# Kernel tuning notes

Measured on AMD Instinct MI355X. Metric: run time of the kernel, lower is better.

Reference implementation:

```python
import jax, jax.numpy as jnp
import numpy as np

# Longformer-base-like config, 4 layers, seq 2048, one-sided window 256 (attention_window=512)
B, S, DM, H, L, FF, V, WIN = 1, 2048, 768, 12, 4, 3072, 50265, 256


def _ln(x, s, b):
    m = x.mean(-1, keepdims=True)
    v = ((x - m) ** 2).mean(-1, keepdims=True)
    return (x - m) * jax.lax.rsqrt(v + 1e-5) * s + b


def setup_inputs() -> dict:
    key = jax.random.key(0)
    ks = iter(jax.random.split(key, 48))
    nrm = lambda shape: jax.random.normal(next(ks), shape, jnp.float32) * 0.02
    z = lambda shape: jnp.zeros(shape, jnp.float32)
    o = lambda shape: jnp.ones(shape, jnp.float32)
    return {
        'src': jax.random.randint(next(ks), (B, S), 0, V),
        'mask_src': jnp.ones((B, S), jnp.int32),
        'cluster_sizes': jax.random.randint(next(ks), (B,), 1, 10),
        'emb_word': nrm((V, DM)), 'emb_pos': nrm((S + 2, DM)),
        'ln_emb_s': o((DM,)), 'ln_emb_b': z((DM,)),
        'Wq': nrm((L, DM, DM)), 'bq': z((L, DM)),
        'Wk': nrm((L, DM, DM)), 'bk': z((L, DM)),
        'Wv': nrm((L, DM, DM)), 'bv': z((L, DM)),
        'Wo': nrm((L, DM, DM)), 'bo': z((L, DM)),
        'Wqg': nrm((L, DM, DM)), 'bqg': z((L, DM)),
        'Wkg': nrm((L, DM, DM)), 'bkg': z((L, DM)),
        'Wvg': nrm((L, DM, DM)), 'bvg': z((L, DM)),
        'ln1_s': o((L, DM)), 'ln1_b': z((L, DM)),
        'Wff1': nrm((L, DM, FF)), 'bff1': z((L, FF)),
        'Wff2': nrm((L, FF, DM)), 'bff2': z((L, DM)),
        'ln2_s': o((L, DM)), 'ln2_b': z((L, DM)),
        'Wcls': nrm((DM,)), 'bcls': z(()),
    }


def _encode(src, mask_src, emb_word, emb_pos, ln_emb_s, ln_emb_b,
            Wq, bq, Wk, bk, Wv, bv, Wo, bo, Wqg, bqg, Wkg, bkg, Wvg, bvg,
            ln1_s, ln1_b, Wff1, bff1, Wff2, bff2, ln2_s, ln2_b):
    Dh = DM // H
    NC = S // WIN  # number of query chunks
    NEG = jnp.float32(-1e9)
    scale = jnp.float32(1.0 / np.sqrt(Dh))
    mask_f = mask_src.astype(jnp.float32)

    # RoBERTa-style embeddings (positions offset by padding_idx+1 = 2)
    x = _ln(emb_word[src] + emb_pos[jnp.arange(S) + 2][None], ln_emb_s, ln_emb_b)

    # Banded gather indices: chunk c of W queries sees 3W keys [c*W - W, c*W + 2W)
    idx = jnp.arange(NC)[:, None] * WIN + jnp.arange(3 * WIN)[None, :]  # [NC,3W] into padded seq
    j_abs = idx - WIN                                                   # absolute key positions
    qi = jnp.arange(NC)[:, None] * WIN + jnp.arange(WIN)[None, :]       # [NC,W] absolute query pos
    rel = j_abs[:, None, :] - qi[:, :, None]                            # [NC,W,3W]
    in_band = (jnp.abs(rel) <= WIN) & (j_abs[:, None, :] >= 0) & (j_abs[:, None, :] < S)
    # keys removed from windowed attention: padding tokens and global tokens (position 0)
    key_ok = mask_f * (jnp.arange(S)[None, :] != 0)                     # [B,S]
    kmb = jnp.pad(key_ok, ((0, 0), (WIN, WIN)))[:, idx]                 # [B,NC,3W]
    band_ok = in_band[None, None] & (kmb[:, None, :, None, :] > 0)      # [B,1,NC,W,3W]

    for l in range(L):
        heads = lambda Wm, bm: (x @ Wm[l] + bm[l]).reshape(B, S, H, Dh).transpose(0, 2, 1, 3)
        q = heads(Wq, bq) * scale                                       # [B,H,S,Dh]
        k = heads(Wk, bk)
        v = heads(Wv, bv)
        kb = jnp.pad(k, ((0, 0), (0, 0), (WIN, WIN), (0, 0)))[:, :, idx]  # [B,H,NC,3W,Dh]
        vb = jnp.pad(v, ((0, 0), (0, 0), (WIN, WIN), (0, 0)))[:, :, idx]
        band = jnp.einsum('bhcqd,bhckd->bhcqk', q.reshape(B, H, NC, WIN, Dh), kb)
        band = jnp.where(band_ok, band, NEG)
        # every query also attends the global key (position 0) via the regular k/v
        sg = jnp.einsum('bhsd,bhd->bhs', q, k[:, :, 0])
        sg = jnp.where((mask_f[:, 0] > 0)[:, None, None], sg, NEG).reshape(B, H, NC, WIN, 1)
        probs = jax.nn.softmax(jnp.concatenate([sg, band], axis=-1), axis=-1)
        pg = probs[..., 0].reshape(B, H, S)
        out = jnp.einsum('bhcqk,bhckd->bhcqd', probs[..., 1:], vb).reshape(B, H, S, Dh)
        out = out + pg[..., None] * v[:, :, 0][:, :, None, :]
        # global query token (position 0): full attention using the *_global projections
        qg = ((x[:, 0] @ Wqg[l] + bqg[l]).reshape(B, H, Dh)) * scale
        kg = heads(Wkg, bkg)
        vg = heads(Wvg, bvg)
        sgl = jnp.where(mask_f[:, None, :] > 0, jnp.einsum('bhd,bhsd->bhs', qg, kg), NEG)
        og = jnp.einsum('bhs,bhsd->bhd', jax.nn.softmax(sgl, axis=-1), vg)
        out = out.at[:, :, 0].set(og)
        ctx = out.transpose(0, 2, 1, 3).reshape(B, S, DM)
        x = _ln(x + ctx @ Wo[l] + bo[l], ln1_s[l], ln1_b[l])
        ff = jax.nn.gelu(x @ Wff1[l] + bff1[l], approximate=False) @ Wff2[l] + bff2[l]
        x = _ln(x + ff, ln2_s[l], ln2_b[l])
    return x


def reference(src, mask_src, cluster_sizes, emb_word, emb_pos, ln_emb_s, ln_emb_b,
              Wq, bq, Wk, bk, Wv, bv, Wo, bo, Wqg, bqg, Wkg, bkg, Wvg, bvg,
              ln1_s, ln1_b, Wff1, bff1, Wff2, bff2, ln2_s, ln2_b, Wcls, bcls):
    x = _encode(src, mask_src, emb_word, emb_pos, ln_emb_s, ln_emb_b,
                Wq, bq, Wk, bk, Wv, bv, Wo, bo, Wqg, bqg, Wkg, bkg, Wvg, bvg,
                ln1_s, ln1_b, Wff1, bff1, Wff2, bff2, ln2_s, ln2_b)
    mask0 = mask_src[:, 0].astype(jnp.float32)
    scores = jax.nn.sigmoid(x[:, 0] @ Wcls + bcls) * mask0  # Classifier on CLS embedding
    return scores[:, None], mask_src[:, 0][:, None]
```

## Files before the change

### kernel.cpp

```cpp
#include <hip/hip_runtime.h>
#include <hip/hip_bf16.h>
#include <math.h>

#define S_LEN 2048
#define DMODEL 768
#define NHEAD 12
#define DHEAD 64
#define NLAYER 4
#define FFDIM 3072
#define WINSZ 256

typedef unsigned short u16;
typedef __attribute__((ext_vector_type(8))) short bfrag;
typedef __attribute__((ext_vector_type(4))) float ffrag;

static __device__ __forceinline__ int detect_bf16(const unsigned* flagp) {
    return flagp[0] != 0x3F800000u;
}

static __device__ __forceinline__ float ldin(const void* p, long i, int bf) {
    return bf ? __bfloat162float(((const __hip_bfloat16*)p)[i])
              : ((const float*)p)[i];
}

static __device__ __forceinline__ u16 f2bf(float v) {
    unsigned u = __float_as_uint(v);
    unsigned r = (u + 0x7FFFu + ((u >> 16) & 1u)) >> 16;
    return (u16)r;
}

static __device__ __forceinline__ float bf2f(u16 v) {
    return __uint_as_float((unsigned)v << 16);
}

static __device__ __forceinline__ void async16(const u16* g, u16* l) {
#if __has_builtin(__builtin_amdgcn_global_load_lds)
    __builtin_amdgcn_global_load_lds(
        (const __attribute__((address_space(1))) void*)g,
        (__attribute__((address_space(3))) void*)l, 16, 0, 0);
#else
    *(int4*)l = *(const int4*)g;
#endif
}

static __device__ __forceinline__ void blk_reduce_sum2(float& a, float& b) {
    __shared__ float sred[8];
    #pragma unroll
    for (int off = 32; off; off >>= 1) {
        a += __shfl_down(a, off);
        b += __shfl_down(b, off);
    }
    int lane = threadIdx.x & 63, w = threadIdx.x >> 6;
    if (lane == 0) { sred[w] = a; sred[w + 4] = b; }
    __syncthreads();
    a = sred[0] + sred[1] + sred[2] + sred[3];
    b = sred[4] + sred[5] + sred[6] + sred[7];
    __syncthreads();
}

struct TAllArgs { const void* w[8]; u16* d6; u16* d1; u16* d2; };

__global__ __launch_bounds__(256)
void transpose_all_kernel(TAllArgs args, const unsigned* __restrict__ flagp) {
    int bf = detect_bf16(flagp);
    const long DD = (long)DMODEL * DMODEL;
    const long DF = (long)DMODEL * FFDIM;
    int bid = blockIdx.x;
    const void* srcp; u16* dst; int K, N, n0, k0; long so, dofs;
    if (bid < 3456) {
        int z = bid / 144, t = bid % 144;
        srcp = args.w[z >> 2]; so = (long)(z & 3) * DD;
        dst = args.d6; dofs = (long)z * DD;
        K = DMODEL; N = DMODEL; n0 = (t % 12) * 64; k0 = (t / 12) * 64;
    } else if (bid < 5760) {
        int i = bid - 3456, layer = i / 576, t = i % 576;
        srcp = args.w[6]; so = (long)layer * DF;
        dst = args.d1; dofs = (long)layer * DF;
        K = DMODEL; N = FFDIM; n0 = (t % 48) * 64; k0 = (t / 48) * 64;
    } else {
        int i = bid - 5760, layer = i / 576, t = i % 576;
        srcp = args.w[7]; so = (long)layer * DF;
        dst = args.d2; dofs = (long)layer * DF;
        K = FFDIM; N = DMODEL; n0 = (t % 12) * 64; k0 = (t / 12) * 64;
    }
    __shared__ float t[64][65];
    int tid = threadIdx.x;
    #pragma unroll
    for (int r = 0; r < 16; ++r) {
        int idx = r * 256 + tid;
        int k = idx >> 6, n = idx & 63;
        t[k][n] = ldin(srcp, so + (long)(k0 + k) * N + n0 + n, bf);
    }
    __syncthreads();
    #pragma unroll
    for (int r = 0; r < 4; ++r) {
        int idx = r * 256 + tid;
        int n = idx >> 4, k4 = (idx & 15) * 4;
        ushort4 pk;
        pk.x = f2bf(t[k4 + 0][n]); pk.y = f2bf(t[k4 + 1][n]);
        pk.z = f2bf(t[k4 + 2][n]); pk.w = f2bf(t[k4 + 3][n]);
        *(ushort4*)&dst[dofs + (long)(n0 + n) * K + k0 + k4] = pk;
    }
}

__global__ __launch_bounds__(256)
void embed_kernel(const int* __restrict__ src, const void* __restrict__ emb_word,
                  const void* __restrict__ emb_pos, const void* __restrict__ ln_s,
                  const void* __restrict__ ln_b, float* __restrict__ X,
                  u16* __restrict__ Xb, const unsigned* __restrict__ flagp) {
    int bf = detect_bf16(flagp);
    int s = blockIdx.x;
    int tid = threadIdx.x;
    int tok = src[s];
    float e[3];
    #pragma unroll
    for (int i = 0; i < 3; ++i) {
        int d = tid + i * 256;
        e[i] = ldin(emb_word, (long)tok * DMODEL + d, bf)
             + ldin(emb_pos, (long)(s + 2) * DMODEL + d, bf);
    }
    float sum = e[0] + e[1] + e[2];
    float sq  = e[0]*e[0] + e[1]*e[1] + e[2]*e[2];
    blk_reduce_sum2(sum, sq);
    float mean = sum * (1.0f / DMODEL);
    float var  = sq * (1.0f / DMODEL) - mean * mean;
    float inv  = rsqrtf(var + 1e-5f);
    #pragma unroll
    for (int i = 0; i < 3; ++i) {
        int d = tid + i * 256;
        float v = (e[i] - mean) * inv * ldin(ln_s, d, bf) + ldin(ln_b, d, bf);
        X[(long)s * DMODEL + d] = v;
        Xb[(long)s * DMODEL + d] = f2bf(v);
    }
}

__global__ __launch_bounds__(256)
void ln_res2_kernel(float* __restrict__ X, const float* __restrict__ T0,
                    const float* __restrict__ T1,
                    const void* __restrict__ ln_s, long soff,
                    const void* __restrict__ ln_b, long boff,
                    u16* __restrict__ Xb, const unsigned* __restrict__ flagp,
                    int do_cls, const void* __restrict__ Wcls,
                    const void* __restrict__ bcls, const int* __restrict__ mask_src,
                    void* __restrict__ out) {
    int bf = detect_bf16(flagp);
    int s = blockIdx.x;
    int tid = threadIdx.x;
    float e[3];
    #pragma unroll
    for (int i = 0; i < 3; ++i) {
        long d = (long)s * DMODEL + tid + i * 256;
        e[i] = X[d] + T0[d] + T1[d];
    }
    float sum = e[0] + e[1] + e[2];
    float sq  = e[0]*e[0] + e[1]*e[1] + e[2]*e[2];
    blk_reduce_sum2(sum, sq);
    float mean = sum * (1.0f / DMODEL);
    float var  = sq * (1.0f / DMODEL) - mean * mean;
    float inv  = rsqrtf(var + 1e-5f);
    float v3[3];
    #pragma unroll
    for (int i = 0; i < 3; ++i) {
        int d = tid + i * 256;
        float v = (e[i] - mean) * inv * ldin(ln_s, soff + d, bf) + ldin(ln_b, boff + d, bf);
        v3[i] = v;
        X[(long)s * DMODEL + d] = v;
        Xb[(long)s * DMODEL + d] = f2bf(v);
    }
    if (do_cls && s == 0) {
        float a = 0.0f, dummy = 0.0f;
        #pragma unroll
        for (int i = 0; i < 3; ++i)
            a = fmaf(v3[i], ldin(Wcls, tid + i * 256, bf), a);
        blk_reduce_sum2(a, dummy);
        if (tid == 0) {
            float z = a + ldin(bcls, 0, bf);
            float scr = 1.0f / (1.0f + __expf(-z));
            float mk = (float)mask_src[0];
            scr *= mk;
            if (bf) {
                __hip_bfloat16* o = (__hip_bfloat16*)out;
                o[0] = __float2bfloat16(scr);
                o[1] = __float2bfloat16(mk);
            } else {
                float* o = (float*)out;
                o[0] = scr;
                o[1] = mk;
            }
        }
    }
}

static __device__ __forceinline__ void gemm_body(
    const u16* __restrict__ A, int lda, const u16* __restrict__ Wt, int ldb,
    const void* __restrict__ bias, long boff, int bf,
    float* __restrict__ outF, u16* __restrict__ outB, u16* __restrict__ outBT, int ldt,
    int N, int klen, float alpha, int gelu,
    u16 (*As)[32], u16 (*Bs)[32], int bm, int bn,
    int patch_mode, const u16* __restrict__ ctx0s, long kbeg)
{
    int tid = threadIdx.x;
    int wave = tid >> 6, lane = tid & 63;
    int quad = lane >> 4, l15 = lane & 15;
    int wn = wave * 32;

    int srow = tid >> 2;
    int scol = (tid & 3) * 8;
    const u16* Ag  = A  + (long)(bm + srow) * lda + scol;
    const u16* Bg0 = Wt + (long)(bn + srow) * ldb + scol;
    const u16* Bg1 = Wt + (long)(bn + 64 + srow) * ldb + scol;
    u16* Al  = &As[srow][scol];
    u16* Bl0 = &Bs[srow][scol];
    u16* Bl1 = &Bs[64 + srow][scol];

    ffrag zero = {0.f, 0.f, 0.f, 0.f};
    ffrag acc[4][2];
    #pragma unroll
    for (int mi = 0; mi < 4; ++mi)
        #pragma unroll
        for (int ni = 0; ni < 2; ++ni) acc[mi][ni] = zero;

    for (int k0 = 0; k0 < klen; k0 += 32) {
        __syncthreads();
        async16(Ag + k0, Al);
        async16(Bg0 + k0, Bl0);
        async16(Bg1 + k0, Bl1);
        __syncthreads();
        if (patch_mode) {
            if (bm == 0 && tid < 4) {
                #pragma unroll
                for (int j = 0; j < 8; ++j)
                    As[0][tid * 8 + j] = ctx0s[kbeg + k0 + tid * 8 + j];
            }
            __syncthreads();
        }
        bfrag af[4], bfr[2];
        #pragma unroll
        for (int mi = 0; mi < 4; ++mi)
            af[mi] = *(const bfrag*)&As[mi * 16 + l15][quad * 8];
        #pragma unroll
        for (int ni = 0; ni < 2; ++ni)
            bfr[ni] = *(const bfrag*)&Bs[wn + ni * 16 + l15][quad * 8];
        #pragma unroll
        for (int mi = 0; mi < 4; ++mi)
            #pragma unroll
            for (int ni = 0; ni < 2; ++ni)
                acc[mi][ni] = __builtin_amdgcn_mfma_f32_16x16x32_bf16(
                    af[mi], bfr[ni], acc[mi][ni], 0, 0, 0);
    }

    #pragma unroll
    for (int mi = 0; mi < 4; ++mi) {
        #pragma unroll
        for (int ni = 0; ni < 2; ++ni) {
            int row0 = bm + mi * 16 + quad * 4;
            int col  = bn + wn + ni * 16 + l15;
            float bb = bias ? ldin(bias, boff + col, bf) : 0.0f;
            float v[4];
            #pragma unroll
            for (int i = 0; i < 4; ++i) {
                float x = (acc[mi][ni][i] + bb) * alpha;
                if (gelu) x = 0.5f * x * (1.0f + erff(x * 0.70710678118f));
                v[i] = x;
            }
            if (outF) {
                #pragma unroll
                for (int i = 0; i < 4; ++i) outF[(long)(row0 + i) * N + col] = v[i];
            }
            if (outB) {
                #pragma unroll
                for (int i = 0; i < 4; ++i) outB[(long)(row0 + i) * N + col] = f2bf(v[i]);
            }
            if (outBT) {
                ushort4 pk;
                pk.x = f2bf(v[0]); pk.y = f2bf(v[1]); pk.z = f2bf(v[2]); pk.w = f2bf(v[3]);
                *(ushort4*)&outBT[(long)col * ldt + row0] = pk;
            }
        }
    }
}

__global__ __launch_bounds__(256)
void gemm_one_kernel(const u16* __restrict__ A, int lda, const u16* __restrict__ Wt, int ldb,
                     const void* __restrict__ bias, long boff,
                     float* __restrict__ outF, long ofstride, u16* __restrict__ outB,
                     int N, int klen, float alpha, int gelu,
                     const float* __restrict__ Gml, const float* __restrict__ GO,
                     const unsigned* __restrict__ flagp) {
    __shared__ __align__(16) u16 As[64][32];
    __shared__ __align__(16) u16 Bs[128][32];
    __shared__ __align__(16) u16 ctx0s[DMODEL];
    int patch = (Gml != nullptr);
    int bm = blockIdx.x * 64;
    if (patch && bm == 0) {
        for (int i = threadIdx.x; i < DMODEL; i += 256) {
            int h = i >> 6, d = i & 63;
            float M = -3e38f;
            #pragma unroll
            for (int z = 0; z < 8; ++z) M = fmaxf(M, Gml[((long)h * 8 + z) * 2]);
            float L = 0.f, O = 0.f;
            #pragma unroll
            for (int z = 0; z < 8; ++z) {
                float w = __expf(Gml[((long)h * 8 + z) * 2] - M);
                L += Gml[((long)h * 8 + z) * 2 + 1] * w;
                O = fmaf(GO[((long)h * 8 + z) * DHEAD + d], w, O);
            }
            ctx0s[i] = f2bf(O / L);
        }
    }
    long kbeg = (long)blockIdx.z * klen;
    gemm_body(A + kbeg, lda, Wt + kbeg, ldb,
              blockIdx.z == 0 ? bias : nullptr, boff, detect_bf16(flagp),
              outF ? outF + blockIdx.z * ofstride : nullptr, outB, nullptr, 0,
              N, klen, alpha, gelu, As, Bs, bm, blockIdx.y * 128,
              patch, ctx0s, kbeg);
}

struct Qkv5Args {
    const u16* wt[5];
    const void* bias[5];
    u16* outB[5];
    u16* outBT[5];
};

__global__ __launch_bounds__(256)
void gemm_qkv5_kernel(const u16* __restrict__ A, Qkv5Args args, long boff,
                      const unsigned* __restrict__ flagp) {
    __shared__ __align__(16) u16 As[64][32];
    __shared__ __align__(16) u16 Bs[128][32];
    int z = blockIdx.z;
    float alpha = (z == 0) ? 0.125f : 1.0f;
    gemm_body(A, DMODEL, args.wt[z], DMODEL, args.bias[z], boff, detect_bf16(flagp),
              nullptr, args.outB[z], args.outBT[z], S_LEN,
              DMODEL, DMODEL, alpha, 0,
              As, Bs, blockIdx.x * 64, blockIdx.y * 128, 0, nullptr, 0);
}

struct BandShared {
    u16 Qs[64][72];
    u16 Ks[64][72];
    u16 Vs[64][72];
    float Pb[4][16][68];
    u16 k0s[64];
    u16 v0s[64];
};
struct GattnShared {
    float xs[DMODEL];
    float qs[DHEAD];
    float sc[256];
    float red[4];
    float pt[4][DHEAD];
};
union AttnShared { BandShared b; GattnShared g; };

__global__ __launch_bounds__(256)
void attn_fused_kernel(const u16* __restrict__ Qb, const u16* __restrict__ Kb,
                       const u16* __restrict__ Vtg, u16* __restrict__ CTXb,
                       const float* __restrict__ X, const void* __restrict__ Wqg, long wo,
                       const void* __restrict__ bqg, long bo,
                       const u16* __restrict__ KG, const u16* __restrict__ VG,
                       float* __restrict__ Gml, float* __restrict__ GO,
                       const unsigned* __restrict__ flagp) {
    __shared__ __align__(16) AttnShared sm;
    int bid = blockIdx.x;
    int tid = threadIdx.x;

    if (bid < 384) {
        int qt = bid & 31, h = bid >> 5;
        int q0 = qt * 64;
        int wave = tid >> 6, lane = tid & 63;
        int quad = lane >> 4, l15 = lane & 15;

        {
            int r = tid >> 2, seg = tid & 3;
            const u16* gq = Qb + (long)(q0 + r) * DMODEL + h * DHEAD + seg * 16;
            *(int4*)&sm.b.Qs[r][seg * 16]     = *(const int4*)gq;
            *(int4*)&sm.b.Qs[r][seg * 16 + 8] = *(const int4*)(gq + 8);
            if (tid < 8) *(int4*)&sm.b.k0s[tid * 8] = *(const int4*)(Kb + h * DHEAD + tid * 8);
            if (tid >= 64 && tid < 128) {
                int d = tid - 64;
                sm.b.v0s[d] = Vtg[(long)(h * DHEAD + d) * S_LEN];
            }
        }
        __syncthreads();

        float part = 0.0f;
        #pragma unroll
        for (int j = 0; j < 16; ++j)
            part = fmaf(bf2f(sm.b.Qs[wave * 16 + l15][quad * 16 + j]),
                        bf2f(sm.b.k0s[quad * 16 + j]), part);
        part += __shfl_xor(part, 16);
        part += __shfl_xor(part, 32);
        float m = part, l = 1.0f;

        ffrag O4[4];
        #pragma unroll
        for (int dt = 0; dt < 4; ++dt) {
            float vv = bf2f(sm.b.v0s[dt * 16 + l15]);
            ffrag t = {vv, vv, vv, vv};
            O4[dt] = t;
        }

        bfrag bq[2];
        bq[0] = *(const bfrag*)&sm.b.Qs[wave * 16 + l15][quad * 8];
        bq[1] = *(const bfrag*)&sm.b.Qs[wave * 16 + l15][32 + quad * 8];

        int q_abs = q0 + wave * 16 + l15;
        float (*Pw)[68] = sm.b.Pb[wave];

        for (int t = 0; t < 9; ++t) {
            int jb = q0 - 256 + t * 64;
            if (jb < 0 || jb >= S_LEN) continue;

            __syncthreads();
            {
                int r = tid >> 2, seg = tid & 3;
                const u16* gk = Kb + (long)(jb + r) * DMODEL + h * DHEAD + seg * 16;
                *(int4*)&sm.b.Ks[r][seg * 16]     = *(const int4*)gk;
                *(int4*)&sm.b.Ks[r][seg * 16 + 8] = *(const int4*)(gk + 8);
                const u16* gv = Vtg + (long)(h * DHEAD + r) * S_LEN + jb + seg * 16;
                *(int4*)&sm.b.Vs[r][seg * 16]     = *(const int4*)gv;
                *(int4*)&sm.b.Vs[r][seg * 16 + 8] = *(const int4*)(gv + 8);
            }
            __syncthreads();

            ffrag sa[4];
            #pragma unroll
            for (int mt = 0; mt < 4; ++mt) {
                bfrag a0 = *(const bfrag*)&sm.b.Ks[mt * 16 + l15][quad * 8];
                bfrag a1 = *(const bfrag*)&sm.b.Ks[mt * 16 + l15][32 + quad * 8];
                ffrag z = {0.f, 0.f, 0.f, 0.f};
                z = __builtin_amdgcn_mfma_f32_16x16x32_bf16(a0, bq[0], z, 0, 0, 0);
                z = __builtin_amdgcn_mfma_f32_16x16x32_bf16(a1, bq[1], z, 0, 0, 0);
                sa[mt] = z;
            }

            float mx = -3e38f;
            #pragma unroll
            for (int mt = 0; mt < 4; ++mt) {
                #pragma unroll
                for (int reg = 0; reg < 4; ++reg) {
                    int key = jb + mt * 16 + quad * 4 + reg;
                    int rel = key - q_abs;
                    bool ok = (key >= 1) && (rel >= -WINSZ) && (rel <= WINSZ);
                    float s = ok ? sa[mt][reg] : -1e30f;
                    sa[mt][reg] = s;
                    mx = fmaxf(mx, s);
                }
            }
            mx = fmaxf(mx, __shfl_xor(mx, 16));
            mx = fmaxf(mx, __shfl_xor(mx, 32));
            float m_new = fmaxf(m, mx);
            float alpha = __expf(m - m_new);

            float rs = 0.0f;
            #pragma unroll
            for (int mt = 0; mt < 4; ++mt) {
                #pragma unroll
                for (int reg = 0; reg < 4; ++reg) {
                    float p = __expf(sa[mt][reg] - m_new);
                    sa[mt][reg] = p;
                    rs += p;
                }
            }
            rs += __shfl_xor(rs, 16);
            rs += __shfl_xor(rs, 32);
            l = l * alpha + rs;
            m = m_new;

            #pragma unroll
            for (int mt = 0; mt < 4; ++mt)
                #pragma unroll
                for (int reg = 0; reg < 4; ++reg)
                    Pw[l15][mt * 16 + quad * 4 + reg] = sa[mt][reg];

            float a4[4];
            #pragma unroll
            for (int reg = 0; reg < 4; ++reg)
                a4[reg] = __shfl(alpha, (lane & 48) + quad * 4 + reg);

            bfrag pa[2];
            #pragma unroll
            for (int ks = 0; ks < 2; ++ks) {
                float4 f0 = *(const float4*)&Pw[l15][ks * 32 + quad * 8];
                float4 f1 = *(const float4*)&Pw[l15][ks * 32 + quad * 8 + 4];
                union { bfrag v; short s[8]; } pu;
                pu.s[0] = (short)f2bf(f0.x); pu.s[1] = (short)f2bf(f0.y);
                pu.s[2] = (short)f2bf(f0.z); pu.s[3] = (short)f2bf(f0.w);
                pu.s[4] = (short)f2bf(f1.x); pu.s[5] = (short)f2bf(f1.y);
                pu.s[6] = (short)f2bf(f1.z); pu.s[7] = (short)f2bf(f1.w);
                pa[ks] = pu.v;
            }

            #pragma unroll
            for (int dt = 0; dt < 4; ++dt) {
                bfrag v0f = *(const bfrag*)&sm.b.Vs[dt * 16 + l15][quad * 8];
                bfrag v1f = *(const bfrag*)&sm.b.Vs[dt * 16 + l15][32 + quad * 8];
                ffrag o = O4[dt];
                #pragma unroll
                for (int reg = 0; reg < 4; ++reg) o[reg] *= a4[reg];
                o = __builtin_amdgcn_mfma_f32_16x16x32_bf16(pa[0], v0f, o, 0, 0, 0);
                o = __builtin_amdgcn_mfma_f32_16x16x32_bf16(pa[1], v1f, o, 0, 0, 0);
                O4[dt] = o;
            }
        }

        float l4[4];
        #pragma unroll
        for (int reg = 0; reg < 4; ++reg)
            l4[reg] = __shfl(l, (lane & 48) + quad * 4 + reg);

        #pragma unroll
        for (int dt = 0; dt < 4; ++dt) {
            #pragma unroll
            for (int reg = 0; reg < 4; ++reg) {
                int row = q0 + wave * 16 + quad * 4 + reg;
                CTXb[(long)row * DMODEL + h * DHEAD + dt * 16 + l15] = f2bf(O4[dt][reg] / l4[reg]);
            }
        }
    } else {
        int bf = detect_bf16(flagp);
        int idx = bid - 384;
        int h = idx >> 3, ck = idx & 7;

        for (int i = tid; i < DMODEL; i += 256) sm.g.xs[i] = X[i];
        __syncthreads();
        {
            int d = tid & 63, part = tid >> 6;
            float a = 0.0f;
            for (int k = part * 192; k < part * 192 + 192; ++k)
                a = fmaf(sm.g.xs[k], ldin(Wqg, wo + (long)k * DMODEL + h * DHEAD + d, bf), a);
            sm.g.pt[part][d] = a;
        }
        __syncthreads();
        if (tid < DHEAD)
            sm.g.qs[tid] = ((sm.g.pt[0][tid] + sm.g.pt[1][tid] + sm.g.pt[2][tid] + sm.g.pt[3][tid])
                            + ldin(bqg, bo + h * DHEAD + tid, bf)) * 0.125f;
        __syncthreads();

        int s = ck * 256 + tid;
        const int4* kp = (const int4*)(KG + (long)s * DMODEL + h * DHEAD);
        float dsum = 0.0f;
        #pragma unroll
        for (int i = 0; i < 8; ++i) {
            int4 raw = kp[i];
            const u16* pr = (const u16*)&raw;
            #pragma unroll
            for (int j = 0; j < 8; ++j) dsum = fmaf(sm.g.qs[i * 8 + j], bf2f(pr[j]), dsum);
        }
        sm.g.sc[tid] = dsum;
        float v = dsum;
        #pragma unroll
        for (int off = 32; off; off >>= 1) v = fmaxf(v, __shfl_down(v, off));
        if ((tid & 63) == 0) sm.g.red[tid >> 6] = v;
        __syncthreads();
        float M = fmaxf(fmaxf(sm.g.red[0], sm.g.red[1]), fmaxf(sm.g.red[2], sm.g.red[3]));
        __syncthreads();
        float e = __expf(dsum - M);
        sm.g.sc[tid] = e;
        float sum = e;
        #pragma unroll
        for (int off = 32; off; off >>= 1) sum += __shfl_down(sum, off);
        if ((tid & 63) == 0) sm.g.red[tid >> 6] = sum;
        __syncthreads();
        float L = sm.g.red[0] + sm.g.red[1] + sm.g.red[2] + sm.g.red[3];

        int g = tid >> 6, dd = tid & 63;
        float acc = 0.0f;
        for (int j = g * 64; j < g * 64 + 64; ++j)
            acc = fmaf(sm.g.sc[j], bf2f(VG[(long)(ck * 256 + j) * DMODEL + h * DHEAD + dd]), acc);
        sm.g.pt[g][dd] = acc;
        __syncthreads();
        if (tid < DHEAD)
            GO[((long)h * 8 + ck) * DHEAD + tid] =
                sm.g.pt[0][tid] + sm.g.pt[1][tid] + sm.g.pt[2][tid] + sm.g.pt[3][tid];
        if (tid == 0) {
            Gml[((long)h * 8 + ck) * 2]     = M;
            Gml[((long)h * 8 + ck) * 2 + 1] = L;
        }
    }
}

extern "C" void kernel_launch(void* const* d_in, const int* in_sizes, int n_in,
                              void* d_out, int out_size, void* d_ws, size_t ws_size,
                              hipStream_t stream) {
    (void)in_sizes; (void)n_in; (void)out_size; (void)ws_size;
    const int* src       = (const int*)d_in[0];
    const int* mask_src  = (const int*)d_in[1];
    const void* emb_word = d_in[3];
    const void* emb_pos  = d_in[4];
    const unsigned* flagp = (const unsigned*)d_in[5];
    const void* ln_emb_s = d_in[5];
    const void* ln_emb_b = d_in[6];

    char* base = (char*)d_ws;
    size_t off = 0;
    auto carve = [&](size_t bytes) {
        void* p = base + off;
        off = (off + bytes + 255) & ~(size_t)255;
        return p;
    };
    const long DD = (long)DMODEL * DMODEL;
    const long DF = (long)DMODEL * FFDIM;
    const long SD = (long)S_LEN * DMODEL;
    const long SF = (long)S_LEN * FFDIM;

    u16* W6    = (u16*)carve(6 * NLAYER * DD * 2);
    u16* FF1T  = (u16*)carve(NLAYER * DF * 2);
    u16* FF2T  = (u16*)carve(NLAYER * DF * 2);
    float* X   = (float*)carve(SD * 4);
    float* TMP0 = (float*)carve(SD * 4);
    float* TMP1 = (float*)carve(SD * 4);
    u16* Xb    = (u16*)carve(SD * 2);
    u16* Qb16  = (u16*)carve(SD * 2);
    u16* Kb16  = (u16*)carve(SD * 2);
    u16* Vtg   = (u16*)carve(SD * 2);
    u16* KGb16 = (u16*)carve(SD * 2);
    u16* VGb16 = (u16*)carve(SD * 2);
    u16* CTXb  = (u16*)carve(SD * 2);
    u16* FF1b  = (u16*)carve(SF * 2);
    float* Gml = (float*)carve(NHEAD * 8 * 2 * 4);
    float* GO  = (float*)carve(NHEAD * 8 * DHEAD * 4);

    TAllArgs ta;
    ta.w[0] = d_in[7];  ta.w[1] = d_in[9];  ta.w[2] = d_in[11];
    ta.w[3] = d_in[17]; ta.w[4] = d_in[19]; ta.w[5] = d_in[13];
    ta.w[6] = d_in[23]; ta.w[7] = d_in[25];
    ta.d6 = W6; ta.d1 = FF1T; ta.d2 = FF2T;
    transpose_all_kernel<<<8064, 256, 0, stream>>>(ta, flagp);

    embed_kernel<<<S_LEN, 256, 0, stream>>>(src, emb_word, emb_pos, ln_emb_s, ln_emb_b,
                                            X, Xb, flagp);

    for (int l = 0; l < NLAYER; ++l) {
        long wo  = (long)l * DD;
        long bo  = (long)l * DMODEL;
        long b1o = (long)l * FFDIM;

        Qkv5Args qa;
        qa.wt[0] = W6 + (0L * NLAYER + l) * DD; qa.bias[0] = d_in[8];  qa.outB[0] = Qb16;  qa.outBT[0] = nullptr;
        qa.wt[1] = W6 + (1L * NLAYER + l) * DD; qa.bias[1] = d_in[10]; qa.outB[1] = Kb16;  qa.outBT[1] = nullptr;
        qa.wt[2] = W6 + (2L * NLAYER + l) * DD; qa.bias[2] = d_in[12]; qa.outB[2] = nullptr; qa.outBT[2] = Vtg;
        qa.wt[3] = W6 + (3L * NLAYER + l) * DD; qa.bias[3] = d_in[18]; qa.outB[3] = KGb16; qa.outBT[3] = nullptr;
        qa.wt[4] = W6 + (4L * NLAYER + l) * DD; qa.bias[4] = d_in[20]; qa.outB[4] = VGb16; qa.outBT[4] = nullptr;
        gemm_qkv5_kernel<<<dim3(32, 6, 5), 256, 0, stream>>>(Xb, qa, bo, flagp);

        attn_fused_kernel<<<480, 256, 0, stream>>>(Qb16, Kb16, Vtg, CTXb,
                                                   X, d_in[15], wo, d_in[16], bo,
                                                   KGb16, VGb16, Gml, GO, flagp);

        gemm_one_kernel<<<dim3(32, 6, 2), 256, 0, stream>>>(
            CTXb, DMODEL, W6 + (5L * NLAYER + l) * DD, DMODEL, d_in[14], bo,
            TMP0, SD, nullptr, DMODEL, 384, 1.0f, 0, Gml, GO, flagp);
        ln_res2_kernel<<<S_LEN, 256, 0, stream>>>(X, TMP0, TMP1, d_in[21], bo, d_in[22], bo,
                                                  Xb, flagp, 0, nullptr, nullptr, nullptr, nullptr);

        gemm_one_kernel<<<dim3(32, 24, 1), 256, 0, stream>>>(
            Xb, DMODEL, FF1T + (long)l * DF, DMODEL, d_in[24], b1o,
            nullptr, 0, FF1b, FFDIM, DMODEL, 1.0f, 1, nullptr, nullptr, flagp);
        gemm_one_kernel<<<dim3(32, 6, 2), 256, 0, stream>>>(
            FF1b, FFDIM, FF2T + (long)l * DF, FFDIM, d_in[26], bo,
            TMP0, SD, nullptr, DMODEL, 1536, 1.0f, 0, nullptr, nullptr, flagp);
        ln_res2_kernel<<<S_LEN, 256, 0, stream>>>(X, TMP0, TMP1, d_in[27], bo, d_in[28], bo,
                                                  Xb, flagp, (l == NLAYER - 1) ? 1 : 0,
                                                  d_in[29], d_in[30], mask_src, d_out);
    }
}
```

Before: 973.7 us.

## Double-buffer GEMM LDS tiles, enlarge to 128x128 per block, vectorize transpose loads

The shared GEMM body now uses 128x128 output tiles with a 2x2 wave layout (4x4 MFMA fragments per wave) in place of 64x128. LDS tiles are double-buffered so the async global-to-LDS copy of the next K slice overlaps the MFMAs on the current one, with a single waitcnt/barrier per iteration. The patch row for the global-attention context is injected straight into the A fragment registers. The weight-transpose prep kernel also switches to 4-wide vector loads. Together these aim to raise data reuse and hide load latency. In exchange they halve the grid size, so fewer blocks are available to fill the CUs, and LDS use per block grows.

Result: slower. 1.039 ms (+6.7%).

```diff
diff --git a/kernel.cpp b/kernel.cpp
--- a/kernel.cpp
+++ b/kernel.cpp
@@ -86,10 +86,19 @@
     __shared__ float t[64][65];
     int tid = threadIdx.x;
     #pragma unroll
-    for (int r = 0; r < 16; ++r) {
+    for (int r = 0; r < 4; ++r) {
         int idx = r * 256 + tid;
-        int k = idx >> 6, n = idx & 63;
-        t[k][n] = ldin(srcp, so + (long)(k0 + k) * N + n0 + n, bf);
+        int k = idx >> 4, n4 = (idx & 15) * 4;
+        long sidx = so + (long)(k0 + k) * N + n0 + n4;
+        if (bf) {
+            ushort4 u = *(const ushort4*)((const u16*)srcp + sidx);
+            t[k][n4 + 0] = bf2f(u.x); t[k][n4 + 1] = bf2f(u.y);
+            t[k][n4 + 2] = bf2f(u.z); t[k][n4 + 3] = bf2f(u.w);
+        } else {
+            float4 vv = *(const float4*)((const float*)srcp + sidx);
+            t[k][n4 + 0] = vv.x; t[k][n4 + 1] = vv.y;
+            t[k][n4 + 2] = vv.z; t[k][n4 + 3] = vv.w;
+        }
     }
     __syncthreads();
     #pragma unroll
@@ -191,70 +200,81 @@
     }
 }
 
+typedef u16 lds_tile[128][32];
+
 static __device__ __forceinline__ void gemm_body(
     const u16* __restrict__ A, int lda, const u16* __restrict__ Wt, int ldb,
     const void* __restrict__ bias, long boff, int bf,
     float* __restrict__ outF, u16* __restrict__ outB, u16* __restrict__ outBT, int ldt,
     int N, int klen, float alpha, int gelu,
-    u16 (*As)[32], u16 (*Bs)[32], int bm, int bn,
+    lds_tile* As2, lds_tile* Bs2, int bm, int bn,
     int patch_mode, const u16* __restrict__ ctx0s, long kbeg)
 {
     int tid = threadIdx.x;
     int wave = tid >> 6, lane = tid & 63;
     int quad = lane >> 4, l15 = lane & 15;
-    int wn = wave * 32;
+    int wr = wave >> 1, wc = wave & 1;
 
     int srow = tid >> 2;
     int scol = (tid & 3) * 8;
-    const u16* Ag  = A  + (long)(bm + srow) * lda + scol;
+    const u16* Ag0 = A  + (long)(bm + srow) * lda + scol;
+    const u16* Ag1 = A  + (long)(bm + 64 + srow) * lda + scol;
     const u16* Bg0 = Wt + (long)(bn + srow) * ldb + scol;
     const u16* Bg1 = Wt + (long)(bn + 64 + srow) * ldb + scol;
-    u16* Al  = &As[srow][scol];
-    u16* Bl0 = &Bs[srow][scol];
-    u16* Bl1 = &Bs[64 + srow][scol];
 
     ffrag zero = {0.f, 0.f, 0.f, 0.f};
-    ffrag acc[4][2];
+    ffrag acc[4][4];
     #pragma unroll
     for (int mi = 0; mi < 4; ++mi)
         #pragma unroll
-        for (int ni = 0; ni < 2; ++ni) acc[mi][ni] = zero;
-
-    for (int k0 = 0; k0 < klen; k0 += 32) {
-        __syncthreads();
-        async16(Ag + k0, Al);
-        async16(Bg0 + k0, Bl0);
-        async16(Bg1 + k0, Bl1);
-        __syncthreads();
-        if (patch_mode) {
-            if (bm == 0 && tid < 4) {
-                #pragma unroll
-                for (int j = 0; j < 8; ++j)
-                    As[0][tid * 8 + j] = ctx0s[kbeg + k0 + tid * 8 + j];
-            }
-            __syncthreads();
-        }
-        bfrag af[4], bfr[2];
+        for (int ni = 0; ni < 4; ++ni) acc[mi][ni] = zero;
+
+    async16(Ag0, &As2[0][srow][scol]);
+    async16(Ag1, &As2[0][64 + srow][scol]);
+    async16(Bg0, &Bs2[0][srow][scol]);
+    async16(Bg1, &Bs2[0][64 + srow][scol]);
+    asm volatile("s_waitcnt vmcnt(0)" ::: "memory");
+    __builtin_amdgcn_s_barrier();
+
+    int nt = klen >> 5;
+    for (int t = 0; t < nt; ++t) {
+        int cur = t & 1;
+        if (t + 1 < nt) {
+            int kn = (t + 1) << 5;
+            async16(Ag0 + kn, &As2[cur ^ 1][srow][scol]);
+            async16(Ag1 + kn, &As2[cur ^ 1][64 + srow][scol]);
+            async16(Bg0 + kn, &Bs2[cur ^ 1][srow][scol]);
+            async16(Bg1 + kn, &Bs2[cur ^ 1][64 + srow][scol]);
+        }
+        int k0 = t << 5;
+        bfrag af[4], bfr[4];
         #pragma unroll
         for (int mi = 0; mi < 4; ++mi)
-            af[mi] = *(const bfrag*)&As[mi * 16 + l15][quad * 8];
-        #pragma unroll
-        for (int ni = 0; ni < 2; ++ni)
-            bfr[ni] = *(const bfrag*)&Bs[wn + ni * 16 + l15][quad * 8];
+            af[mi] = *(const bfrag*)&As2[cur][wr * 64 + mi * 16 + l15][quad * 8];
+        if (patch_mode && bm == 0) {
+            bfrag cf = *(const bfrag*)&ctx0s[kbeg + k0 + quad * 8];
+            bool pr = (wr == 0) && (l15 == 0);
+            af[0] = pr ? cf : af[0];
+        }
+        #pragma unroll
+        for (int ni = 0; ni < 4; ++ni)
+            bfr[ni] = *(const bfrag*)&Bs2[cur][wc * 64 + ni * 16 + l15][quad * 8];
         #pragma unroll
         for (int mi = 0; mi < 4; ++mi)
             #pragma unroll
-            for (int ni = 0; ni < 2; ++ni)
+            for (int ni = 0; ni < 4; ++ni)
                 acc[mi][ni] = __builtin_amdgcn_mfma_f32_16x16x32_bf16(
                     af[mi], bfr[ni], acc[mi][ni], 0, 0, 0);
+        asm volatile("s_waitcnt vmcnt(0)" ::: "memory");
+        __builtin_amdgcn_s_barrier();
     }
 
     #pragma unroll
     for (int mi = 0; mi < 4; ++mi) {
         #pragma unroll
-        for (int ni = 0; ni < 2; ++ni) {
-            int row0 = bm + mi * 16 + quad * 4;
-            int col  = bn + wn + ni * 16 + l15;
+        for (int ni = 0; ni < 4; ++ni) {
+            int row0 = bm + wr * 64 + mi * 16 + quad * 4;
+            int col  = bn + wc * 64 + ni * 16 + l15;
             float bb = bias ? ldin(bias, boff + col, bf) : 0.0f;
             float v[4];
             #pragma unroll
@@ -287,11 +307,11 @@
                      int N, int klen, float alpha, int gelu,
                      const float* __restrict__ Gml, const float* __restrict__ GO,
                      const unsigned* __restrict__ flagp) {
-    __shared__ __align__(16) u16 As[64][32];
-    __shared__ __align__(16) u16 Bs[128][32];
+    __shared__ __align__(16) u16 As[2][128][32];
+    __shared__ __align__(16) u16 Bs[2][128][32];
     __shared__ __align__(16) u16 ctx0s[DMODEL];
     int patch = (Gml != nullptr);
-    int bm = blockIdx.x * 64;
+    int bm = blockIdx.x * 128;
     if (patch && bm == 0) {
         for (int i = threadIdx.x; i < DMODEL; i += 256) {
             int h = i >> 6, d = i & 63;
@@ -326,14 +346,14 @@
 __global__ __launch_bounds__(256)
 void gemm_qkv5_kernel(const u16* __restrict__ A, Qkv5Args args, long boff,
                       const unsigned* __restrict__ flagp) {
-    __shared__ __align__(16) u16 As[64][32];
-    __shared__ __align__(16) u16 Bs[128][32];
+    __shared__ __align__(16) u16 As[2][128][32];
+    __shared__ __align__(16) u16 Bs[2][128][32];
     int z = blockIdx.z;
     float alpha = (z == 0) ? 0.125f : 1.0f;
     gemm_body(A, DMODEL, args.wt[z], DMODEL, args.bias[z], boff, detect_bf16(flagp),
               nullptr, args.outB[z], args.outBT[z], S_LEN,
               DMODEL, DMODEL, alpha, 0,
-              As, Bs, blockIdx.x * 64, blockIdx.y * 128, 0, nullptr, 0);
+              As, Bs, blockIdx.x * 128, blockIdx.y * 128, 0, nullptr, 0);
 }
 
 struct BandShared {
@@ -643,22 +663,22 @@
         qa.wt[2] = W6 + (2L * NLAYER + l) * DD; qa.bias[2] = d_in[12]; qa.outB[2] = nullptr; qa.outBT[2] = Vtg;
         qa.wt[3] = W6 + (3L * NLAYER + l) * DD; qa.bias[3] = d_in[18]; qa.outB[3] = KGb16; qa.outBT[3] = nullptr;
         qa.wt[4] = W6 + (4L * NLAYER + l) * DD; qa.bias[4] = d_in[20]; qa.outB[4] = VGb16; qa.outBT[4] = nullptr;
-        gemm_qkv5_kernel<<<dim3(32, 6, 5), 256, 0, stream>>>(Xb, qa, bo, flagp);
+        gemm_qkv5_kernel<<<dim3(16, 6, 5), 256, 0, stream>>>(Xb, qa, bo, flagp);
 
         attn_fused_kernel<<<480, 256, 0, stream>>>(Qb16, Kb16, Vtg, CTXb,
                                                    X, d_in[15], wo, d_in[16], bo,
                                                    KGb16, VGb16, Gml, GO, flagp);
 
-        gemm_one_kernel<<<dim3(32, 6, 2), 256, 0, stream>>>(
+        gemm_one_kernel<<<dim3(16, 6, 2), 256, 0, stream>>>(
             CTXb, DMODEL, W6 + (5L * NLAYER + l) * DD, DMODEL, d_in[14], bo,
             TMP0, SD, nullptr, DMODEL, 384, 1.0f, 0, Gml, GO, flagp);
         ln_res2_kernel<<<S_LEN, 256, 0, stream>>>(X, TMP0, TMP1, d_in[21], bo, d_in[22], bo,
                                                   Xb, flagp, 0, nullptr, nullptr, nullptr, nullptr);
 
-        gemm_one_kernel<<<dim3(32, 24, 1), 256, 0, stream>>>(
+        gemm_one_kernel<<<dim3(16, 24, 1), 256, 0, stream>>>(
             Xb, DMODEL, FF1T + (long)l * DF, DMODEL, d_in[24], b1o,
             nullptr, 0, FF1b, FFDIM, DMODEL, 1.0f, 1, nullptr, nullptr, flagp);
-        gemm_one_kernel<<<dim3(32, 6, 2), 256, 0, stream>>>(
+        gemm_one_kernel<<<dim3(16, 6, 2), 256, 0, stream>>>(
             FF1b, FFDIM, FF2T + (long)l * DF, FFDIM, d_in[26], bo,
             TMP0, SD, nullptr, DMODEL, 1536, 1.0f, 0, nullptr, nullptr, flagp);
         ln_res2_kernel<<<S_LEN, 256, 0, stream>>>(X, TMP0, TMP1, d_in[27], bo, d_in[28], bo,
```

## Triple-buffer GEMM LDS tiles with async prefetch and vectorize weight transpose loads

Applied to the files above, without the earlier changes.

The GEMM main loop moves from a single LDS buffer with two barriers per k-step to a three-stage ring buffer. It prefetches two tiles ahead and uses explicit vmcnt waits with one barrier per step. The ctx0 patch for row 0 is now applied in registers instead of by rewriting LDS with an extra barrier. The weight transpose prep kernel also switches to vectorized 4-wide global loads. The cost is three times the LDS per block, which may lower occupancy, and the hand-tuned waitcnt counts could be fragile.

After: 971.0 us. About the same (-0.3%).

```diff
diff --git a/kernel.cpp b/kernel.cpp
--- a/kernel.cpp
+++ b/kernel.cpp
@@ -86,10 +86,19 @@
     __shared__ float t[64][65];
     int tid = threadIdx.x;
     #pragma unroll
-    for (int r = 0; r < 16; ++r) {
+    for (int r = 0; r < 4; ++r) {
         int idx = r * 256 + tid;
-        int k = idx >> 6, n = idx & 63;
-        t[k][n] = ldin(srcp, so + (long)(k0 + k) * N + n0 + n, bf);
+        int k = idx >> 4, n4 = (idx & 15) * 4;
+        long sidx = so + (long)(k0 + k) * N + n0 + n4;
+        if (bf) {
+            ushort4 u = *(const ushort4*)((const u16*)srcp + sidx);
+            t[k][n4 + 0] = bf2f(u.x); t[k][n4 + 1] = bf2f(u.y);
+            t[k][n4 + 2] = bf2f(u.z); t[k][n4 + 3] = bf2f(u.w);
+        } else {
+            float4 vv = *(const float4*)((const float*)srcp + sidx);
+            t[k][n4 + 0] = vv.x; t[k][n4 + 1] = vv.y;
+            t[k][n4 + 2] = vv.z; t[k][n4 + 3] = vv.w;
+        }
     }
     __syncthreads();
     #pragma unroll
@@ -191,12 +200,15 @@
     }
 }
 
+typedef u16 ldsA_t[64][32];
+typedef u16 ldsB_t[128][32];
+
 static __device__ __forceinline__ void gemm_body(
     const u16* __restrict__ A, int lda, const u16* __restrict__ Wt, int ldb,
     const void* __restrict__ bias, long boff, int bf,
     float* __restrict__ outF, u16* __restrict__ outB, u16* __restrict__ outBT, int ldt,
     int N, int klen, float alpha, int gelu,
-    u16 (*As)[32], u16 (*Bs)[32], int bm, int bn,
+    ldsA_t* As2, ldsB_t* Bs2, int bm, int bn,
     int patch_mode, const u16* __restrict__ ctx0s, long kbeg)
 {
     int tid = threadIdx.x;
@@ -209,9 +221,6 @@
     const u16* Ag  = A  + (long)(bm + srow) * lda + scol;
     const u16* Bg0 = Wt + (long)(bn + srow) * ldb + scol;
     const u16* Bg1 = Wt + (long)(bn + 64 + srow) * ldb + scol;
-    u16* Al  = &As[srow][scol];
-    u16* Bl0 = &Bs[srow][scol];
-    u16* Bl1 = &Bs[64 + srow][scol];
 
     ffrag zero = {0.f, 0.f, 0.f, 0.f};
     ffrag acc[4][2];
@@ -220,33 +229,45 @@
         #pragma unroll
         for (int ni = 0; ni < 2; ++ni) acc[mi][ni] = zero;
 
-    for (int k0 = 0; k0 < klen; k0 += 32) {
-        __syncthreads();
-        async16(Ag + k0, Al);
-        async16(Bg0 + k0, Bl0);
-        async16(Bg1 + k0, Bl1);
-        __syncthreads();
-        if (patch_mode) {
-            if (bm == 0 && tid < 4) {
-                #pragma unroll
-                for (int j = 0; j < 8; ++j)
-                    As[0][tid * 8 + j] = ctx0s[kbeg + k0 + tid * 8 + j];
-            }
-            __syncthreads();
+    async16(Ag,       &As2[0][srow][scol]);
+    async16(Bg0,      &Bs2[0][srow][scol]);
+    async16(Bg1,      &Bs2[0][64 + srow][scol]);
+    async16(Ag + 32,  &As2[1][srow][scol]);
+    async16(Bg0 + 32, &Bs2[1][srow][scol]);
+    async16(Bg1 + 32, &Bs2[1][64 + srow][scol]);
+    __syncthreads();
+
+    int nt = klen >> 5;
+    int cw = 0, iw = 2;
+    for (int t = 0; t < nt; ++t) {
+        if (t + 2 < nt) {
+            int kn = (t + 2) << 5;
+            async16(Ag + kn,  &As2[iw][srow][scol]);
+            async16(Bg0 + kn, &Bs2[iw][srow][scol]);
+            async16(Bg1 + kn, &Bs2[iw][64 + srow][scol]);
         }
         bfrag af[4], bfr[2];
         #pragma unroll
         for (int mi = 0; mi < 4; ++mi)
-            af[mi] = *(const bfrag*)&As[mi * 16 + l15][quad * 8];
+            af[mi] = *(const bfrag*)&As2[cw][mi * 16 + l15][quad * 8];
+        if (patch_mode && bm == 0) {
+            bfrag cf = *(const bfrag*)&ctx0s[kbeg + (t << 5) + quad * 8];
+            af[0] = (l15 == 0) ? cf : af[0];
+        }
         #pragma unroll
         for (int ni = 0; ni < 2; ++ni)
-            bfr[ni] = *(const bfrag*)&Bs[wn + ni * 16 + l15][quad * 8];
+            bfr[ni] = *(const bfrag*)&Bs2[cw][wn + ni * 16 + l15][quad * 8];
         #pragma unroll
         for (int mi = 0; mi < 4; ++mi)
             #pragma unroll
             for (int ni = 0; ni < 2; ++ni)
                 acc[mi][ni] = __builtin_amdgcn_mfma_f32_16x16x32_bf16(
                     af[mi], bfr[ni], acc[mi][ni], 0, 0, 0);
+        if (t + 2 < nt) asm volatile("s_waitcnt vmcnt(3)" ::: "memory");
+        else            asm volatile("s_waitcnt vmcnt(0)" ::: "memory");
+        __builtin_amdgcn_s_barrier();
+        cw = (cw == 2) ? 0 : cw + 1;
+        iw = (iw == 2) ? 0 : iw + 1;
     }
 
     #pragma unroll
@@ -287,8 +308,8 @@
                      int N, int klen, float alpha, int gelu,
                      const float* __restrict__ Gml, const float* __restrict__ GO,
                      const unsigned* __restrict__ flagp) {
-    __shared__ __align__(16) u16 As[64][32];
-    __shared__ __align__(16) u16 Bs[128][32];
+    __shared__ __align__(16) u16 As[3][64][32];
+    __shared__ __align__(16) u16 Bs[3][128][32];
     __shared__ __align__(16) u16 ctx0s[DMODEL];
     int patch = (Gml != nullptr);
     int bm = blockIdx.x * 64;
@@ -326,8 +347,8 @@
 __global__ __launch_bounds__(256)
 void gemm_qkv5_kernel(const u16* __restrict__ A, Qkv5Args args, long boff,
                       const unsigned* __restrict__ flagp) {
-    __shared__ __align__(16) u16 As[64][32];
-    __shared__ __align__(16) u16 Bs[128][32];
+    __shared__ __align__(16) u16 As[3][64][32];
+    __shared__ __align__(16) u16 Bs[3][128][32];
     int z = blockIdx.z;
     float alpha = (z == 0) ? 0.125f : 1.0f;
     gemm_body(A, DMODEL, args.wt[z], DMODEL, args.bias[z], boff, detect_bf16(flagp),
```
